# Optimization experiments

Hardware: AMD Instinct MI355X
Metric: run time of the kernel (lower is better)

The kernel has to match this reference:

```python
import jax, jax.numpy as jnp
import numpy as np


def setup_inputs() -> dict:
    key = jax.random.key(0)
    ks = jax.random.split(key, 8)
    B, S, Ta, D = 64, 512, 8, 768
    return {
        "memory": jax.random.normal(ks[0], (B, S, D), dtype=jnp.float32),
        "aspect_states": jax.random.normal(ks[1], (B, Ta, D), dtype=jnp.float32),
        "input_ids": jnp.ones((B, S), dtype=jnp.int64),
        "input_t_ids": jnp.ones((B, Ta), dtype=jnp.int64),
        "W1": jax.random.normal(ks[2], (3 * D, D), dtype=jnp.float32) * 0.02,
        "b1": jnp.zeros((D,), dtype=jnp.float32),
        "w2": jax.random.normal(ks[3], (D,), dtype=jnp.float32) * 0.02,
        "Wm": jax.random.normal(ks[4], (D, D), dtype=jnp.float32) * 0.02,
        "bm": jnp.zeros((D,), dtype=jnp.float32),
        "Wd": jax.random.normal(ks[5], (D, 3), dtype=jnp.float32) * 0.02,
        "bd": jnp.zeros((3,), dtype=jnp.float32),
    }


def reference(memory, aspect_states, input_ids, input_t_ids, W1, b1, w2, Wm, bm, Wd, bd):
    B, S, D = memory.shape
    memory_len = jnp.sum(input_ids != 0, axis=-1)          # [B]
    aspect_len = jnp.sum(input_t_ids != 0, axis=-1)        # [B]

    # v_a: mean-pooled aspect representation  [B, D]
    v_a = jnp.sum(aspect_states, axis=1) / aspect_len.astype(memory.dtype)[:, None]
    # v_s: mean-pooled sentence representation [B, D]
    v_s = jnp.sum(memory, axis=1) / memory_len.astype(memory.dtype)[:, None]

    # locationed_memory: memory[i, idx] *= 1 - idx/memory_len[i] for idx < memory_len[i]
    idx = jnp.arange(S, dtype=memory.dtype)                 # [S]
    mlen = memory_len.astype(memory.dtype)[:, None]         # [B, 1]
    loc = jnp.where(idx[None, :] < mlen, 1.0 - idx[None, :] / mlen, 1.0)  # [B, S]
    memory = memory * loc[:, :, None]

    # chunked linear1/linear2 scorer, vectorized:
    # c_t = w2 . tanh(W1 @ [m_t ; v_a ; v_s] + b1)
    W1_m, W1_a, W1_s = W1[:D], W1[D:2 * D], W1[2 * D:]
    ctx = v_a @ W1_a + v_s @ W1_s + b1                      # [B, D]
    h = jnp.tanh(jnp.einsum("bsd,de->bse", memory, W1_m) + ctx[:, None, :])
    scores = h @ w2                                         # [B, S]
    alpha = jax.nn.softmax(scores, axis=1)

    v_ts = jnp.einsum("bsd,bs->bd", memory, alpha)          # [B, D]
    v_ns = v_ts + v_s
    v_ms = jnp.tanh(v_ns @ Wm + bm)
    logits = v_ms @ Wd + bd                                 # [B, 3]
    return logits
```

## Files before the change

kernel.cpp:

```cpp
#include <hip/hip_runtime.h>
#include <hip/hip_bf16.h>


#define NB 64
#define NS 512
#define ND 768
#define NTA 8

typedef __attribute__((ext_vector_type(8))) __bf16 bf16x8;
typedef __attribute__((ext_vector_type(4))) float f32x4;

#define OFF_SCORES 0u
#define OFF_VS 131072u
#define OFF_VTS 327680u
#define OFF_CTX 524288u
#define OFF_U 720896u
#define ZERO_BYTES 917504u
#define OFF_VA 917504u
#define OFF_LENS 1114112u
#define OFF_W1MT 1115136u
#define OFF_MP 2294784u

__device__ __forceinline__ float fast_tanh(float x) {
  x = fminf(fmaxf(x, -15.f), 15.f);
  float t = __expf(2.f * x);
  return __fdividef(t - 1.f, t + 1.f);
}

__device__ __forceinline__ unsigned bfpack2(float a, float b) {
  unsigned ua = __float_as_uint(a), ub = __float_as_uint(b);
  ua = (ua + 0x7FFFu + ((ua >> 16) & 1u)) >> 16;
  ub = (ub + 0x7FFFu + ((ub >> 16) & 1u)) >> 16;
  return ua | (ub << 16);
}

__device__ __forceinline__ unsigned short bf16b(float f) {
  unsigned u = __float_as_uint(f);
  u = (u + 0x7FFFu + ((u >> 16) & 1u)) >> 16;
  return (unsigned short)u;
}

__device__ __forceinline__ void async_copy16(const void* g, void* l) {
  __builtin_amdgcn_global_load_lds(
      (const __attribute__((address_space(1))) void*)g,
      (__attribute__((address_space(3))) void*)l, 16, 0, 0);
}

__global__ __launch_bounds__(256) void k_prep_tr(const int* __restrict__ ids,
                                                 const int* __restrict__ tids,
                                                 const float* __restrict__ aspect,
                                                 const float* __restrict__ W1,
                                                 float* __restrict__ v_a,
                                                 float* __restrict__ lens,
                                                 unsigned short* __restrict__ w1mt) {
  int bid = blockIdx.x, tid = threadIdx.x;
  if (bid < 576) {
    __shared__ float tile[32][33];
    int bx = bid % 24, by = bid / 24;
    int tx = tid & 31, ty = tid >> 5;
    for (int j = 0; j < 32; j += 8)
      tile[ty + j][tx] = W1[(size_t)(by * 32 + ty + j) * ND + bx * 32 + tx];
    __syncthreads();
    for (int j = 0; j < 32; j += 8)
      w1mt[(size_t)(bx * 32 + ty + j) * ND + by * 32 + tx] = bf16b(tile[tx][ty + j]);
  } else {
    int b = bid - 576;
    __shared__ int red[256];
    __shared__ float sh_inva;
    int cnt = 0;
    for (int j = tid; j < NS; j += 256) cnt += (ids[b * NS + j] != 0);
    red[tid] = cnt;
    __syncthreads();
    for (int s = 128; s > 0; s >>= 1) {
      if (tid < s) red[tid] += red[tid + s];
      __syncthreads();
    }
    if (tid == 0) {
      int mlen = red[0];
      int acnt = 0;
      for (int t = 0; t < NTA; ++t) acnt += (tids[b * NTA + t] != 0);
      lens[b] = (float)mlen;
      lens[64 + b] = 1.0f / (float)mlen;
      float inva = 1.0f / (float)acnt;
      lens[128 + b] = inva;
      sh_inva = inva;
    }
    __syncthreads();
    float inva = sh_inva;
    for (int j = tid; j < ND; j += 256) {
      float s = 0.f;
      for (int t = 0; t < NTA; ++t) s += aspect[((size_t)b * NTA + t) * ND + j];
      v_a[b * ND + j] = s * inva;
    }
  }
}

__global__ __launch_bounds__(192) void k_vs_mprime(const float* __restrict__ memory,
                                                   const float* __restrict__ lens,
                                                   float* __restrict__ v_s,
                                                   unsigned short* __restrict__ mp) {
  int sc = blockIdx.x, b = blockIdx.y, tid = threadIdx.x;
  int d0 = tid * 4;
  float inv_mlen = lens[64 + b];
  float mlenf = lens[b];
  float s0 = 0, s1 = 0, s2 = 0, s3 = 0;
#pragma unroll 8
  for (int s = 0; s < 32; ++s) {
    int srow = sc * 32 + s;
    size_t row = (size_t)b * NS + srow;
    const float4 v = *(const float4*)(memory + row * ND + d0);
    s0 += v.x; s1 += v.y; s2 += v.z; s3 += v.w;
    float fs = (float)srow;
    float loc = (fs < mlenf) ? 1.0f - fs * inv_mlen : 1.0f;
    uint2 pk;
    pk.x = bfpack2(v.x * loc, v.y * loc);
    pk.y = bfpack2(v.z * loc, v.w * loc);
    *(uint2*)(mp + row * ND + d0) = pk;
  }
  float* p = v_s + b * ND + d0;
  atomicAdd(p + 0, s0 * inv_mlen);
  atomicAdd(p + 1, s1 * inv_mlen);
  atomicAdd(p + 2, s2 * inv_mlen);
  atomicAdd(p + 3, s3 * inv_mlen);
}

__global__ __launch_bounds__(128) void k_ctx(const float* __restrict__ W1,
                                             const float* __restrict__ v_a,
                                             const float* __restrict__ v_s,
                                             float* __restrict__ ctx) {
  int b = blockIdx.x, et = blockIdx.y, dc = blockIdx.z, tid = threadIdx.x;
  __shared__ float vbuf[384];
  for (int j = tid; j < 384; j += 128) {
    int k = dc * 384 + j;
    vbuf[j] = (k < ND) ? v_a[b * ND + k] : v_s[b * ND + (k - ND)];
  }
  __syncthreads();
  int e = et * 128 + tid;
  float acc = 0.f;
  const float* Wk = W1 + (size_t)(ND + dc * 384) * ND + e;
#pragma unroll 8
  for (int j = 0; j < 384; ++j) acc += vbuf[j] * Wk[(size_t)j * ND];
  atomicAdd(&ctx[b * ND + e], acc);
}

__global__ __launch_bounds__(256) void k_gemm_scores(const unsigned short* __restrict__ mp,
                                                     const unsigned short* __restrict__ w1mt,
                                                     const float* __restrict__ ctx,
                                                     const float* __restrict__ b1,
                                                     const float* __restrict__ w2,
                                                     float* __restrict__ scores) {
  __shared__ char lds[65536];
  const int tid = threadIdx.x;
  const int wave = tid >> 6, lane = tid & 63;
  const int bid = blockIdx.x;
  const int swz = (bid & 7) * 192 + (bid >> 3);
  const int rt = swz / 6;
  const int et = swz - rt * 6;
  const int row0 = rt * 128, n0 = et * 128;
  const int b = row0 >> 9;
  const int wm = wave & 1, wn = wave >> 1;

  const int lrow = lane >> 3;
  const int qlog = (lane & 7) ^ lrow;
  const char* Abase = (const char*)mp + (size_t)(row0 + lrow) * (ND * 2) + qlog * 16;
  const char* Bbase = (const char*)w1mt + (size_t)(n0 + lrow) * (ND * 2) + qlog * 16;

  f32x4 acc[4][4];
#pragma unroll
  for (int i = 0; i < 4; ++i)
#pragma unroll
    for (int t = 0; t < 4; ++t) acc[i][t] = (f32x4){0.f, 0.f, 0.f, 0.f};

  const int q2 = lane >> 4, c = lane & 15;
  int offA[4][2], offB[4][2];
#pragma unroll
  for (int i = 0; i < 4; ++i) {
    int ml = wm * 64 + i * 16 + c;
    offA[i][0] = ml * 128 + ((q2 ^ (ml & 7)) * 16);
    offA[i][1] = ml * 128 + (((4 + q2) ^ (ml & 7)) * 16);
    int nl = wn * 64 + i * 16 + c;
    offB[i][0] = nl * 128 + ((q2 ^ (nl & 7)) * 16);
    offB[i][1] = nl * 128 + (((4 + q2) ^ (nl & 7)) * 16);
  }

  auto stage = [&](int bufsel, int kb) {
    char* lA = lds + bufsel * 32768;
    char* lB = lA + 16384;
#pragma unroll
    for (int i = 0; i < 4; ++i) {
      int g = wave * 4 + i;
      async_copy16(Abase + (size_t)g * 8 * (ND * 2) + kb, lA + g * 1024);
      async_copy16(Bbase + (size_t)g * 8 * (ND * 2) + kb, lB + g * 1024);
    }
  };

  stage(0, 0);
  stage(1, 128);

#pragma unroll
  for (int t = 0; t < 12; ++t) {
    if (t < 11) { asm volatile("s_waitcnt vmcnt(8)" ::: "memory"); }
    else        { asm volatile("s_waitcnt vmcnt(0)" ::: "memory"); }
    __builtin_amdgcn_s_barrier();
    __builtin_amdgcn_sched_barrier(0);
    const char* lA = lds + (t & 1) * 32768;
    const char* lB = lA + 16384;
    bf16x8 af[2][4], bfr[2][4];
#pragma unroll
    for (int kk = 0; kk < 2; ++kk)
#pragma unroll
      for (int i = 0; i < 4; ++i) {
        af[kk][i] = *(const bf16x8*)(lA + offA[i][kk]);
        bfr[kk][i] = *(const bf16x8*)(lB + offB[i][kk]);
      }
    __builtin_amdgcn_s_setprio(1);
#pragma unroll
    for (int kk = 0; kk < 2; ++kk)
#pragma unroll
      for (int i = 0; i < 4; ++i)
#pragma unroll
        for (int t2 = 0; t2 < 4; ++t2)
          acc[i][t2] = __builtin_amdgcn_mfma_f32_16x16x32_bf16(af[kk][i], bfr[kk][t2], acc[i][t2], 0, 0, 0);
    __builtin_amdgcn_s_setprio(0);
    asm volatile("s_waitcnt lgkmcnt(0)" ::: "memory");
    __builtin_amdgcn_s_barrier();
    __builtin_amdgcn_sched_barrier(0);
    if (t + 2 < 12) stage(t & 1, (t + 2) * 128);
  }

  float ctxv[4], w2v[4];
#pragma unroll
  for (int t = 0; t < 4; ++t) {
    int n = n0 + wn * 64 + t * 16 + c;
    ctxv[t] = ctx[b * ND + n] + b1[n];
    w2v[t] = w2[n];
  }
#pragma unroll
  for (int i = 0; i < 4; ++i) {
#pragma unroll
    for (int r = 0; r < 4; ++r) {
      float s = 0.f;
#pragma unroll
      for (int t = 0; t < 4; ++t) s += fast_tanh(acc[i][t][r] + ctxv[t]) * w2v[t];
      s += __shfl_xor(s, 1, 64);
      s += __shfl_xor(s, 2, 64);
      s += __shfl_xor(s, 4, 64);
      s += __shfl_xor(s, 8, 64);
      if (c == 0) atomicAdd(&scores[row0 + wm * 64 + i * 16 + q2 * 4 + r], s);
    }
  }
}

__global__ __launch_bounds__(192) void k_vts(const unsigned short* __restrict__ mp,
                                             const float* __restrict__ scores,
                                             float* __restrict__ v_ts) {
  int sc = blockIdx.x, b = blockIdx.y, tid = threadIdx.x;
  int lane = tid & 63, wid = tid >> 6;
  __shared__ float sred[3], sred2[3];
  __shared__ float al[32];
  float v0 = scores[b * NS + tid];
  float v1 = scores[b * NS + tid + 192];
  float v2 = (tid < 128) ? scores[b * NS + tid + 384] : -1e30f;
  float m = fmaxf(fmaxf(v0, v1), v2);
  for (int off = 1; off < 64; off <<= 1) m = fmaxf(m, __shfl_xor(m, off, 64));
  if (lane == 0) sred[wid] = m;
  __syncthreads();
  float M = fmaxf(fmaxf(sred[0], sred[1]), sred[2]);
  float e = __expf(v0 - M) + __expf(v1 - M) + ((tid < 128) ? __expf(v2 - M) : 0.f);
  for (int off = 1; off < 64; off <<= 1) e += __shfl_xor(e, off, 64);
  if (lane == 0) sred2[wid] = e;
  __syncthreads();
  float invS = 1.0f / (sred2[0] + sred2[1] + sred2[2]);
  if (tid < 32) al[tid] = __expf(scores[b * NS + sc * 32 + tid] - M) * invS;
  __syncthreads();

  int d0 = tid * 4;
  float a0 = 0, a1 = 0, a2 = 0, a3 = 0;
#pragma unroll 4
  for (int s = 0; s < 32; ++s) {
    size_t row = (size_t)b * NS + sc * 32 + s;
    uint2 pk = *(const uint2*)(mp + row * ND + d0);
    float a = al[s];
    a0 += a * __uint_as_float(pk.x << 16);
    a1 += a * __uint_as_float(pk.x & 0xFFFF0000u);
    a2 += a * __uint_as_float(pk.y << 16);
    a3 += a * __uint_as_float(pk.y & 0xFFFF0000u);
  }
  float* p = v_ts + b * ND + d0;
  atomicAdd(p + 0, a0);
  atomicAdd(p + 1, a1);
  atomicAdd(p + 2, a2);
  atomicAdd(p + 3, a3);
}

__global__ __launch_bounds__(128) void k_final1(const float* __restrict__ v_ts,
                                                const float* __restrict__ v_s,
                                                const float* __restrict__ Wm,
                                                float* __restrict__ u) {
  int b = blockIdx.x, et = blockIdx.y, dc = blockIdx.z, tid = threadIdx.x;
  __shared__ float vbuf[192];
  for (int j = tid; j < 192; j += 128) {
    int d = dc * 192 + j;
    vbuf[j] = v_ts[b * ND + d] + v_s[b * ND + d];
  }
  __syncthreads();
  int e = et * 128 + tid;
  float acc = 0.f;
  const float* Wk = Wm + (size_t)(dc * 192) * ND + e;
#pragma unroll 8
  for (int j = 0; j < 192; ++j) acc += vbuf[j] * Wk[(size_t)j * ND];
  atomicAdd(&u[b * ND + e], acc);
}

__global__ __launch_bounds__(256) void k_final2(const float* __restrict__ u,
                                                const float* __restrict__ bm,
                                                const float* __restrict__ Wd,
                                                const float* __restrict__ bd,
                                                float* __restrict__ out) {
  int b = blockIdx.x, tid = threadIdx.x;
  int wid = tid >> 6, lane = tid & 63;
  __shared__ float red[4][3];
  float p0 = 0, p1 = 0, p2 = 0;
  for (int e = tid; e < ND; e += 256) {
    float vm = fast_tanh(u[b * ND + e] + bm[e]);
    p0 += vm * Wd[e * 3 + 0];
    p1 += vm * Wd[e * 3 + 1];
    p2 += vm * Wd[e * 3 + 2];
  }
  for (int off = 1; off < 64; off <<= 1) {
    p0 += __shfl_xor(p0, off, 64);
    p1 += __shfl_xor(p1, off, 64);
    p2 += __shfl_xor(p2, off, 64);
  }
  if (lane == 0) { red[wid][0] = p0; red[wid][1] = p1; red[wid][2] = p2; }
  __syncthreads();
  if (tid == 0) {
    out[b * 3 + 0] = red[0][0] + red[1][0] + red[2][0] + red[3][0] + bd[0];
    out[b * 3 + 1] = red[0][1] + red[1][1] + red[2][1] + red[3][1] + bd[1];
    out[b * 3 + 2] = red[0][2] + red[1][2] + red[2][2] + red[3][2] + bd[2];
  }
}

extern "C" void kernel_launch(void* const* d_in, const int* in_sizes, int n_in,
                              void* d_out, int out_size, void* d_ws, size_t ws_size,
                              hipStream_t stream) {
  const float* memory = (const float*)d_in[0];
  const float* aspect = (const float*)d_in[1];
  const int* ids = (const int*)d_in[2];
  const int* tids = (const int*)d_in[3];
  const float* W1 = (const float*)d_in[4];
  const float* b1 = (const float*)d_in[5];
  const float* w2 = (const float*)d_in[6];
  const float* Wm = (const float*)d_in[7];
  const float* bm = (const float*)d_in[8];
  const float* Wd = (const float*)d_in[9];
  const float* bd = (const float*)d_in[10];
  float* out = (float*)d_out;

  char* ws = (char*)d_ws;
  float* scores = (float*)(ws + OFF_SCORES);
  float* v_s = (float*)(ws + OFF_VS);
  float* v_ts = (float*)(ws + OFF_VTS);
  float* ctx = (float*)(ws + OFF_CTX);
  float* u = (float*)(ws + OFF_U);
  float* v_a = (float*)(ws + OFF_VA);
  float* lens = (float*)(ws + OFF_LENS);
  unsigned short* w1mt = (unsigned short*)(ws + OFF_W1MT);
  unsigned short* mp = (unsigned short*)(ws + OFF_MP);

  hipMemsetAsync(ws, 0, ZERO_BYTES, stream);

  k_prep_tr<<<640, 256, 0, stream>>>(ids, tids, aspect, W1, v_a, lens, w1mt);
  k_vs_mprime<<<dim3(16, NB), 192, 0, stream>>>(memory, lens, v_s, mp);
  k_ctx<<<dim3(64, 6, 4), 128, 0, stream>>>(W1, v_a, v_s, ctx);
  k_gemm_scores<<<1536, 256, 0, stream>>>(mp, w1mt, ctx, b1, w2, scores);
  k_vts<<<dim3(16, NB), 192, 0, stream>>>(mp, scores, v_ts);
  k_final1<<<dim3(64, 6, 4), 128, 0, stream>>>(v_ts, v_s, Wm, u);
  k_final2<<<NB, 256, 0, stream>>>(u, bm, Wd, bd, out);
}
```

Measured before the change: 303.8 us.

## Replace atomic accumulations with partial buffers and simplify GEMM pipeline

Every float atomicAdd (v_s, ctx, scores, v_ts, u) is replaced by a write into a per-partition buffer, which the consuming kernel then sums, so the memset and atomic contention go away. This adds an extra k_reduce_vs launch and extra partial reads in downstream kernels. The GEMM loop also drops its hand-tuned two-stage prefetch with vmcnt waits and setprio, and uses a one-ahead stage with __syncthreads instead. That probably weakens the overlap between loads and MFMA work.

```diff
diff --git a/kernel.cpp b/kernel.cpp
--- a/kernel.cpp
+++ b/kernel.cpp
@@ -10,16 +10,16 @@
 typedef __attribute__((ext_vector_type(8))) __bf16 bf16x8;
 typedef __attribute__((ext_vector_type(4))) float f32x4;
 
-#define OFF_SCORES 0u
-#define OFF_VS 131072u
-#define OFF_VTS 327680u
-#define OFF_CTX 524288u
-#define OFF_U 720896u
-#define ZERO_BYTES 917504u
-#define OFF_VA 917504u
-#define OFF_LENS 1114112u
-#define OFF_W1MT 1115136u
-#define OFF_MP 2294784u
+#define OFF_PVS 0u
+#define OFF_PVTS 3145728u
+#define OFF_PCTX 6291456u
+#define OFF_PU 7077888u
+#define OFF_PSC 7864320u
+#define OFF_VS 9437184u
+#define OFF_VA 9633792u
+#define OFF_LENS 9830400u
+#define OFF_W1MT 9831424u
+#define OFF_MP 11011072u
 
 __device__ __forceinline__ float fast_tanh(float x) {
   x = fminf(fmaxf(x, -15.f), 15.f);
@@ -97,7 +97,7 @@
 
 __global__ __launch_bounds__(192) void k_vs_mprime(const float* __restrict__ memory,
                                                    const float* __restrict__ lens,
-                                                   float* __restrict__ v_s,
+                                                   float* __restrict__ part_vs,
                                                    unsigned short* __restrict__ mp) {
   int sc = blockIdx.x, b = blockIdx.y, tid = threadIdx.x;
   int d0 = tid * 4;
@@ -117,17 +117,29 @@
     pk.y = bfpack2(v.z * loc, v.w * loc);
     *(uint2*)(mp + row * ND + d0) = pk;
   }
-  float* p = v_s + b * ND + d0;
-  atomicAdd(p + 0, s0 * inv_mlen);
-  atomicAdd(p + 1, s1 * inv_mlen);
-  atomicAdd(p + 2, s2 * inv_mlen);
-  atomicAdd(p + 3, s3 * inv_mlen);
+  float4 o;
+  o.x = s0 * inv_mlen; o.y = s1 * inv_mlen; o.z = s2 * inv_mlen; o.w = s3 * inv_mlen;
+  *(float4*)(part_vs + ((size_t)sc * NB + b) * ND + d0) = o;
+}
+
+__global__ __launch_bounds__(192) void k_reduce_vs(const float* __restrict__ part_vs,
+                                                   float* __restrict__ v_s) {
+  int b = blockIdx.x, tid = threadIdx.x;
+  int d0 = tid * 4;
+  float a0 = 0, a1 = 0, a2 = 0, a3 = 0;
+#pragma unroll
+  for (int p = 0; p < 16; ++p) {
+    const float4 v = *(const float4*)(part_vs + ((size_t)p * NB + b) * ND + d0);
+    a0 += v.x; a1 += v.y; a2 += v.z; a3 += v.w;
+  }
+  float4 o; o.x = a0; o.y = a1; o.z = a2; o.w = a3;
+  *(float4*)(v_s + b * ND + d0) = o;
 }
 
 __global__ __launch_bounds__(128) void k_ctx(const float* __restrict__ W1,
                                              const float* __restrict__ v_a,
                                              const float* __restrict__ v_s,
-                                             float* __restrict__ ctx) {
+                                             float* __restrict__ ctx_part) {
   int b = blockIdx.x, et = blockIdx.y, dc = blockIdx.z, tid = threadIdx.x;
   __shared__ float vbuf[384];
   for (int j = tid; j < 384; j += 128) {
@@ -140,15 +152,15 @@
   const float* Wk = W1 + (size_t)(ND + dc * 384) * ND + e;
 #pragma unroll 8
   for (int j = 0; j < 384; ++j) acc += vbuf[j] * Wk[(size_t)j * ND];
-  atomicAdd(&ctx[b * ND + e], acc);
+  ctx_part[((size_t)dc * NB + b) * ND + e] = acc;
 }
 
 __global__ __launch_bounds__(256) void k_gemm_scores(const unsigned short* __restrict__ mp,
                                                      const unsigned short* __restrict__ w1mt,
-                                                     const float* __restrict__ ctx,
+                                                     const float* __restrict__ ctx_part,
                                                      const float* __restrict__ b1,
                                                      const float* __restrict__ w2,
-                                                     float* __restrict__ scores) {
+                                                     float* __restrict__ sc_part) {
   __shared__ char lds[65536];
   const int tid = threadIdx.x;
   const int wave = tid >> 6, lane = tid & 63;
@@ -195,15 +207,13 @@
   };
 
   stage(0, 0);
-  stage(1, 128);
-
-#pragma unroll
+  __syncthreads();
+
+  int cur = 0;
+#pragma unroll 2
   for (int t = 0; t < 12; ++t) {
-    if (t < 11) { asm volatile("s_waitcnt vmcnt(8)" ::: "memory"); }
-    else        { asm volatile("s_waitcnt vmcnt(0)" ::: "memory"); }
-    __builtin_amdgcn_s_barrier();
-    __builtin_amdgcn_sched_barrier(0);
-    const char* lA = lds + (t & 1) * 32768;
+    if (t < 11) stage(cur ^ 1, (t + 1) * 128);
+    const char* lA = lds + cur * 32768;
     const char* lB = lA + 16384;
     bf16x8 af[2][4], bfr[2][4];
 #pragma unroll
@@ -213,7 +223,6 @@
         af[kk][i] = *(const bf16x8*)(lA + offA[i][kk]);
         bfr[kk][i] = *(const bf16x8*)(lB + offB[i][kk]);
       }
-    __builtin_amdgcn_s_setprio(1);
 #pragma unroll
     for (int kk = 0; kk < 2; ++kk)
 #pragma unroll
@@ -221,20 +230,21 @@
 #pragma unroll
         for (int t2 = 0; t2 < 4; ++t2)
           acc[i][t2] = __builtin_amdgcn_mfma_f32_16x16x32_bf16(af[kk][i], bfr[kk][t2], acc[i][t2], 0, 0, 0);
-    __builtin_amdgcn_s_setprio(0);
-    asm volatile("s_waitcnt lgkmcnt(0)" ::: "memory");
-    __builtin_amdgcn_s_barrier();
-    __builtin_amdgcn_sched_barrier(0);
-    if (t + 2 < 12) stage(t & 1, (t + 2) * 128);
+    __syncthreads();
+    cur ^= 1;
   }
 
   float ctxv[4], w2v[4];
 #pragma unroll
   for (int t = 0; t < 4; ++t) {
     int n = n0 + wn * 64 + t * 16 + c;
-    ctxv[t] = ctx[b * ND + n] + b1[n];
+    float cx = b1[n];
+#pragma unroll
+    for (int dc = 0; dc < 4; ++dc) cx += ctx_part[((size_t)dc * NB + b) * ND + n];
+    ctxv[t] = cx;
     w2v[t] = w2[n];
   }
+  float* scp = sc_part + (size_t)(et * 2 + wn) * (NB * NS);
 #pragma unroll
   for (int i = 0; i < 4; ++i) {
 #pragma unroll
@@ -246,21 +256,28 @@
       s += __shfl_xor(s, 2, 64);
       s += __shfl_xor(s, 4, 64);
       s += __shfl_xor(s, 8, 64);
-      if (c == 0) atomicAdd(&scores[row0 + wm * 64 + i * 16 + q2 * 4 + r], s);
+      if (c == 0) scp[row0 + wm * 64 + i * 16 + q2 * 4 + r] = s;
     }
   }
 }
 
 __global__ __launch_bounds__(192) void k_vts(const unsigned short* __restrict__ mp,
-                                             const float* __restrict__ scores,
-                                             float* __restrict__ v_ts) {
+                                             const float* __restrict__ sc_part,
+                                             float* __restrict__ part_vts) {
   int sc = blockIdx.x, b = blockIdx.y, tid = threadIdx.x;
   int lane = tid & 63, wid = tid >> 6;
   __shared__ float sred[3], sred2[3];
   __shared__ float al[32];
-  float v0 = scores[b * NS + tid];
-  float v1 = scores[b * NS + tid + 192];
-  float v2 = (tid < 128) ? scores[b * NS + tid + 384] : -1e30f;
+  const float* sp = sc_part + b * NS;
+  float v0 = 0, v1 = 0, v2 = 0;
+#pragma unroll
+  for (int p = 0; p < 12; ++p) {
+    const float* spp = sp + (size_t)p * (NB * NS);
+    v0 += spp[tid];
+    v1 += spp[tid + 192];
+    if (tid < 128) v2 += spp[tid + 384];
+  }
+  if (tid >= 128) v2 = -1e30f;
   float m = fmaxf(fmaxf(v0, v1), v2);
   for (int off = 1; off < 64; off <<= 1) m = fmaxf(m, __shfl_xor(m, off, 64));
   if (lane == 0) sred[wid] = m;
@@ -271,12 +288,17 @@
   if (lane == 0) sred2[wid] = e;
   __syncthreads();
   float invS = 1.0f / (sred2[0] + sred2[1] + sred2[2]);
-  if (tid < 32) al[tid] = __expf(scores[b * NS + sc * 32 + tid] - M) * invS;
+  if (tid < 32) {
+    float sv = 0;
+#pragma unroll
+    for (int p = 0; p < 12; ++p) sv += sp[(size_t)p * (NB * NS) + sc * 32 + tid];
+    al[tid] = __expf(sv - M) * invS;
+  }
   __syncthreads();
 
   int d0 = tid * 4;
   float a0 = 0, a1 = 0, a2 = 0, a3 = 0;
-#pragma unroll 4
+#pragma unroll 8
   for (int s = 0; s < 32; ++s) {
     size_t row = (size_t)b * NS + sc * 32 + s;
     uint2 pk = *(const uint2*)(mp + row * ND + d0);
@@ -286,22 +308,22 @@
     a2 += a * __uint_as_float(pk.y << 16);
     a3 += a * __uint_as_float(pk.y & 0xFFFF0000u);
   }
-  float* p = v_ts + b * ND + d0;
-  atomicAdd(p + 0, a0);
-  atomicAdd(p + 1, a1);
-  atomicAdd(p + 2, a2);
-  atomicAdd(p + 3, a3);
-}
-
-__global__ __launch_bounds__(128) void k_final1(const float* __restrict__ v_ts,
+  float4 o; o.x = a0; o.y = a1; o.z = a2; o.w = a3;
+  *(float4*)(part_vts + ((size_t)sc * NB + b) * ND + d0) = o;
+}
+
+__global__ __launch_bounds__(128) void k_final1(const float* __restrict__ part_vts,
                                                 const float* __restrict__ v_s,
                                                 const float* __restrict__ Wm,
-                                                float* __restrict__ u) {
+                                                float* __restrict__ u_part) {
   int b = blockIdx.x, et = blockIdx.y, dc = blockIdx.z, tid = threadIdx.x;
   __shared__ float vbuf[192];
   for (int j = tid; j < 192; j += 128) {
     int d = dc * 192 + j;
-    vbuf[j] = v_ts[b * ND + d] + v_s[b * ND + d];
+    float v = v_s[b * ND + d];
+#pragma unroll
+    for (int p = 0; p < 16; ++p) v += part_vts[((size_t)p * NB + b) * ND + d];
+    vbuf[j] = v;
   }
   __syncthreads();
   int e = et * 128 + tid;
@@ -309,10 +331,10 @@
   const float* Wk = Wm + (size_t)(dc * 192) * ND + e;
 #pragma unroll 8
   for (int j = 0; j < 192; ++j) acc += vbuf[j] * Wk[(size_t)j * ND];
-  atomicAdd(&u[b * ND + e], acc);
-}
-
-__global__ __launch_bounds__(256) void k_final2(const float* __restrict__ u,
+  u_part[((size_t)dc * NB + b) * ND + e] = acc;
+}
+
+__global__ __launch_bounds__(256) void k_final2(const float* __restrict__ u_part,
                                                 const float* __restrict__ bm,
                                                 const float* __restrict__ Wd,
                                                 const float* __restrict__ bd,
@@ -322,7 +344,10 @@
   __shared__ float red[4][3];
   float p0 = 0, p1 = 0, p2 = 0;
   for (int e = tid; e < ND; e += 256) {
-    float vm = fast_tanh(u[b * ND + e] + bm[e]);
+    float uv = bm[e];
+#pragma unroll
+    for (int dc = 0; dc < 4; ++dc) uv += u_part[((size_t)dc * NB + b) * ND + e];
+    float vm = fast_tanh(uv);
     p0 += vm * Wd[e * 3 + 0];
     p1 += vm * Wd[e * 3 + 1];
     p2 += vm * Wd[e * 3 + 2];
@@ -358,23 +383,24 @@
   float* out = (float*)d_out;
 
   char* ws = (char*)d_ws;
-  float* scores = (float*)(ws + OFF_SCORES);
+  float* part_vs = (float*)(ws + OFF_PVS);
+  float* part_vts = (float*)(ws + OFF_PVTS);
+  float* ctx_part = (float*)(ws + OFF_PCTX);
+  float* u_part = (float*)(ws + OFF_PU);
+  float* sc_part = (float*)(ws + OFF_PSC);
   float* v_s = (float*)(ws + OFF_VS);
-  float* v_ts = (float*)(ws + OFF_VTS);
-  float* ctx = (float*)(ws + OFF_CTX);
-  float* u = (float*)(ws + OFF_U);
   float* v_a = (float*)(ws + OFF_VA);
   float* lens = (float*)(ws + OFF_LENS);
   unsigned short* w1mt = (unsigned short*)(ws + OFF_W1MT);
   unsigned short* mp = (unsigned short*)(ws + OFF_MP);
 
-  hipMemsetAsync(ws, 0, ZERO_BYTES, stream);
 
   k_prep_tr<<<640, 256, 0, stream>>>(ids, tids, aspect, W1, v_a, lens, w1mt);
-  k_vs_mprime<<<dim3(16, NB), 192, 0, stream>>>(memory, lens, v_s, mp);
-  k_ctx<<<dim3(64, 6, 4), 128, 0, stream>>>(W1, v_a, v_s, ctx);
-  k_gemm_scores<<<1536, 256, 0, stream>>>(mp, w1mt, ctx, b1, w2, scores);
-  k_vts<<<dim3(16, NB), 192, 0, stream>>>(mp, scores, v_ts);
-  k_final1<<<dim3(64, 6, 4), 128, 0, stream>>>(v_ts, v_s, Wm, u);
-  k_final2<<<NB, 256, 0, stream>>>(u, bm, Wd, bd, out);
-}
+  k_vs_mprime<<<dim3(16, NB), 192, 0, stream>>>(memory, lens, part_vs, mp);
+  k_reduce_vs<<<NB, 192, 0, stream>>>(part_vs, v_s);
+  k_ctx<<<dim3(64, 6, 4), 128, 0, stream>>>(W1, v_a, v_s, ctx_part);
+  k_gemm_scores<<<1536, 256, 0, stream>>>(mp, w1mt, ctx_part, b1, w2, sc_part);
+  k_vts<<<dim3(16, NB), 192, 0, stream>>>(mp, sc_part, part_vts);
+  k_final1<<<dim3(64, 6, 4), 128, 0, stream>>>(part_vts, v_s, Wm, u_part);
+  k_final2<<<NB, 256, 0, stream>>>(u_part, bm, Wd, bd, out);
+}
```

New measurement: 305.5 us. About the same (+0.6%).
